# Kernel optimization log

Hardware: AMD Instinct MI355X
Metric: run time of the kernel (lower is better)

The kernel has to match this reference:

```python
import jax, jax.numpy as jnp
import numpy as np

N_LAYERS = 24
HID = 512
HEADS = 16
HEAD_DIM = HID // HEADS
CAP = 2048
VOCAB = 1025
EOS = 1024
FF = 2048
PE_LEN = 4096
EPS = 1e-5


def setup_inputs() -> dict:
    key = jax.random.key(0)
    ks = jax.random.split(key, 24)
    g = lambda k, shp, s=0.05: jax.random.normal(k, shp, jnp.float32) * s
    return {
        'last_token': jax.random.randint(ks[0], (1, 1), 0, 1024, dtype=jnp.int32),
        'position_index': jax.random.randint(ks[1], (1,), 0, 1024, dtype=jnp.int32),
        'cache_len': jax.random.randint(ks[2], (1,), 0, 1024, dtype=jnp.int32),
        'k_cache': g(ks[3], (N_LAYERS, 1, CAP, HID)),
        'v_cache': g(ks[4], (N_LAYERS, 1, CAP, HID)),
        'emb_table': g(ks[5], (VOCAB, HID)),
        'pe_table': g(ks[6], (PE_LEN, HID)),
        'x_scale': jnp.ones((1,), jnp.float32),
        'alpha': jnp.ones((1,), jnp.float32),
        'qkv_w_t': g(ks[7], (N_LAYERS, HID, 3 * HID)),
        'qkv_b': g(ks[8], (N_LAYERS, 3 * HID)),
        'out_w_t': g(ks[9], (N_LAYERS, HID, HID)),
        'out_b': g(ks[10], (N_LAYERS, HID)),
        'norm_w1': jnp.ones((N_LAYERS, HID), jnp.float32),
        'norm_b1': jnp.zeros((N_LAYERS, HID), jnp.float32),
        'norm_w2': jnp.ones((N_LAYERS, HID), jnp.float32),
        'norm_b2': jnp.zeros((N_LAYERS, HID), jnp.float32),
        'w1_t': g(ks[11], (N_LAYERS, HID, FF)),
        'b1': g(ks[12], (N_LAYERS, FF)),
        'w2_t': g(ks[13], (N_LAYERS, FF, HID)),
        'b2': g(ks[14], (N_LAYERS, HID)),
        'pred_w': g(ks[15], (VOCAB, HID)),
        'pred_b': g(ks[16], (VOCAB,)),
    }


def _layer_norm(x, w, b):
    mu = jnp.mean(x, axis=-1, keepdims=True)
    var = jnp.mean((x - mu) ** 2, axis=-1, keepdims=True)
    return (x - mu) * jax.lax.rsqrt(var + EPS) * w + b


def _decode_core(xy, cache_len, k_cache, v_cache, qkv_w_t, qkv_b, out_w_t, out_b,
                 norm_w1, norm_b1, norm_w2, norm_b2, w1_t, b1, w2_t, b2):
    B, Q, _ = xy.shape  # [1, 1, HID]
    clen = cache_len.astype(jnp.int32).reshape(1)
    next_len = clen + Q
    positions = jnp.arange(CAP)
    write_mask = (positions == clen)[None, :, None]           # [1, CAP, 1]
    valid = (positions < next_len)[None, :, None]             # [1, CAP, 1]
    inv_attn = (positions >= next_len)[None, None, None, :]   # [1, 1, 1, CAP]

    def layer(x, p):
        qw, qb, ow, ob, nw1, nb1, nw2, nb2, W1, B1, W2, B2, kc, vc = p
        qkv = x @ qw + qb                       # [B, Q, 3*HID]
        q, k, v = jnp.split(qkv, 3, axis=-1)
        # one-hot slot write + zero invalid tail (faithful to _update_cache_slot/_zero_invalid_cache_tail)
        kc = jnp.where(valid, jnp.where(write_mask, k, kc), 0.0)
        vc = jnp.where(valid, jnp.where(write_mask, v, vc), 0.0)
        qh = q.reshape(B, Q, HEADS, HEAD_DIM).transpose(0, 2, 1, 3)
        kh = kc.reshape(B, CAP, HEADS, HEAD_DIM).transpose(0, 2, 1, 3)
        vh = vc.reshape(B, CAP, HEADS, HEAD_DIM).transpose(0, 2, 1, 3)
        scores = jnp.einsum('bhqd,bhkd->bhqk', qh, kh) / jnp.sqrt(jnp.float32(HEAD_DIM))
        scores = jnp.where(inv_attn, jnp.float32(-1e30), scores)
        attn = jax.nn.softmax(scores, axis=-1)
        o = jnp.einsum('bhqk,bhkd->bhqd', attn, vh).transpose(0, 2, 1, 3).reshape(B, Q, HID)
        o = o @ ow + ob
        x = _layer_norm(x + o, nw1, nb1)
        h = jax.nn.relu(x @ W1 + B1) @ W2 + B2
        x = _layer_norm(x + h, nw2, nb2)
        return x, (kc, vc)

    x, (k_out, v_out) = jax.lax.scan(
        layer, xy,
        (qkv_w_t, qkv_b, out_w_t, out_b, norm_w1, norm_b1, norm_w2, norm_b2,
         w1_t, b1, w2_t, b2, k_cache, v_cache))
    return x, k_out, v_out, next_len


def reference(last_token, position_index, cache_len, k_cache, v_cache,
              emb_table, pe_table, x_scale, alpha,
              qkv_w_t, qkv_b, out_w_t, out_b,
              norm_w1, norm_b1, norm_w2, norm_b2,
              w1_t, b1, w2_t, b2, pred_w, pred_b):
    y_emb = emb_table[last_token]                              # [B, Q, HID]
    pos = pe_table[position_index.astype(jnp.int32)][None]     # [1, Q, HID]
    xy = y_emb * x_scale[0] + alpha[0] * pos
    x, k_out, v_out, next_len = _decode_core(
        xy, cache_len, k_cache, v_cache, qkv_w_t, qkv_b, out_w_t, out_b,
        norm_w1, norm_b1, norm_w2, norm_b2, w1_t, b1, w2_t, b2)
    logits = x[:, -1] @ pred_w.T + pred_b                      # [B, VOCAB]
    sampled = jnp.argmax(logits, axis=-1, keepdims=True).astype(jnp.int32)
    eos = (sampled.reshape(-1) == EOS).astype(jnp.int32)
    next_pos = position_index.astype(jnp.int32).reshape(1) + 1
    return (logits, sampled, eos, next_len, next_pos, k_out, v_out)
```

## Files before the change

### kernel.cpp

```cpp
#include <hip/hip_runtime.h>
#include <math.h>

#define NL     24
#define HIDDEN 512
#define H3     1536
#define HD     32
#define CAPCTX 2048
#define FFD    2048
#define NVOCAB 1025
#define GRID   256
#define NT     256
#define EPSLN  1e-5f
#define ISQ    0.17677669529663687f

__device__ __forceinline__ float gld(const float* p){ return __hip_atomic_load(p, __ATOMIC_RELAXED, __HIP_MEMORY_SCOPE_AGENT); }
__device__ __forceinline__ void  gst(float* p, float v){ __hip_atomic_store(p, v, __ATOMIC_RELAXED, __HIP_MEMORY_SCOPE_AGENT); }
__device__ __forceinline__ int   ild(const int* p){ return __hip_atomic_load(p, __ATOMIC_RELAXED, __HIP_MEMORY_SCOPE_AGENT); }
__device__ __forceinline__ void  ist(int* p, int v){ __hip_atomic_store(p, v, __ATOMIC_RELAXED, __HIP_MEMORY_SCOPE_AGENT); }

__device__ __forceinline__ void done_add(int* ctr, int tid){
  __syncthreads();
  if (tid == 0) __hip_atomic_fetch_add(ctr, 1, __ATOMIC_RELAXED, __HIP_MEMORY_SCOPE_AGENT);
}
__device__ __forceinline__ void waitge1(const int* c, int tgt){
  if (threadIdx.x == 0){
    int g = 0;
    while (__hip_atomic_load(c, __ATOMIC_RELAXED, __HIP_MEMORY_SCOPE_AGENT) < tgt){
      if (++g > (1<<25)) break;
    }
  }
  __syncthreads();
}
__device__ __forceinline__ void waitgeN(const int* base, int n, int tgt){
  if ((int)threadIdx.x < n){
    const int* c = base + threadIdx.x*16;
    int g = 0;
    while (__hip_atomic_load(c, __ATOMIC_RELAXED, __HIP_MEMORY_SCOPE_AGENT) < tgt){
      if (++g > (1<<25)) break;
    }
  }
  __syncthreads();
}
#define PIN() asm volatile("" ::: "memory")

#define KVF(kb)   ((kb)*16)
#define HEADC(h)  ((64+(h))*16)
#define FF1G(g)   ((80+(g))*16)
#define PRED_C    (88*16)
#define SLINE(par,h) ((90 + (par)*16 + (h))*16)

struct LdsF { float xn[HIDDEN]; float red[16*17]; float r8[8]; float s16[16]; float h16[16]; };
struct LdsAt{ float xn[HIDDEN]; float q[HD]; float e[128]; float v[128*33]; float red[288]; float r8[8]; float o32[HD]; };
union  Lds  { LdsF f; LdsAt a; };

__device__ __forceinline__ void bsum2(float &a, float &bb, float* lds8, int tid){
  #pragma unroll
  for (int o=32;o;o>>=1){ a += __shfl_down(a,o); bb += __shfl_down(bb,o); }
  __syncthreads();
  if ((tid&63)==0){ int w=tid>>6; lds8[w]=a; lds8[4+w]=bb; }
  __syncthreads();
  a  = lds8[0]+lds8[1]+lds8[2]+lds8[3];
  bb = lds8[4]+lds8[5]+lds8[6]+lds8[7];
  __syncthreads();
}

template<int K>
__device__ __forceinline__ float dotred(const float* w, const float* xn, float* red, int tid){
  const int c = tid & 15, s = tid >> 4;
  float a = 0.f;
  #pragma unroll
  for (int k=0;k<K;k++) a += xn[s + 16*k] * w[k];
  red[s*17 + c] = a;
  __syncthreads();
  float d = 0.f;
  if (s == 0){
    #pragma unroll
    for (int k=0;k<16;k++) d += red[k*17 + c];
  }
  __syncthreads();
  return d;
}

__device__ __forceinline__ void kvcopy(int idx, int T, int l, int clen,
    const float* __restrict__ KC, const float* __restrict__ VC,
    float* KO, float* VO, int tid){
  const int t7 = tid & 127, halfr = tid >> 7;
  const float4 z4 = make_float4(0.f,0.f,0.f,0.f);
  for (int r0 = idx*2; r0 < 4096; r0 += 2*T){
    int r = r0 + halfr;
    int p = r & 2047, isv = r >> 11;
    if (p != clen){
      float4* dst = (float4*)((isv ? VO : KO) + ((size_t)l*CAPCTX + p)*HIDDEN);
      if (p < clen){
        const float4* src = (const float4*)((isv ? VC : KC) + ((size_t)l*CAPCTX + p)*HIDDEN);
        dst[t7] = src[t7];
      } else {
        dst[t7] = z4;
      }
    }
  }
}

__global__ __launch_bounds__(NT, 1)
void t2s_decode(const int* __restrict__ LT, const int* __restrict__ PI, const int* __restrict__ CL,
                const float* __restrict__ KC, const float* __restrict__ VC,
                const float* __restrict__ EMB, const float* __restrict__ PE,
                const float* __restrict__ XSc, const float* __restrict__ ALp,
                const float* __restrict__ QKVW, const float* __restrict__ QKVB,
                const float* __restrict__ OUTW, const float* __restrict__ OUTB,
                const float* __restrict__ NW1, const float* __restrict__ NB1,
                const float* __restrict__ NW2, const float* __restrict__ NB2,
                const float* __restrict__ W1, const float* __restrict__ B1,
                const float* __restrict__ W2, const float* __restrict__ B2,
                const float* __restrict__ PW, const float* __restrict__ PB,
                float* __restrict__ OUT, float* __restrict__ WS)
{
  __shared__ Lds L;
  const int b = blockIdx.x, tid = threadIdx.x;

  int* C = (int*)WS;
  float* F   = WS + 2048;
  float* wop = F;
  float* wf2 = F + 16384;
  float* wx  = F + 24576;
  float* wx1 = F + 25088;
  float* wkv = F + 25600;

  float* KO = OUT + 1029;
  float* VO = KO + (size_t)NL*CAPCTX*HIDDEN;

  const int token = LT[0], posi = PI[0], clen = CL[0], nlen = clen + 1;
  const int nch = (nlen + 127) >> 7;
  const int T_copy = 128 + 16*(8 - nch);

  if (b >= 128){
    const int t = b - 128, h = t & 15, ci = t >> 4;
    const int cstar = clen >> 7;

    if (ci >= nch){
      const int idx = 128 + (ci - nch)*16 + h;
      for (int l=0;l<NL;l++) kvcopy(idx, T_copy, l, clen, KC, VC, KO, VO, tid);
    } else {
      const int c = tid & 31, s5 = tid >> 5;
      const int pl = tid >> 1, half = tid & 1, dbase = half << 4;
      const int p = (ci << 7) + pl;
      const bool validp = (p < nlen);
      const bool isnew  = validp && (p == clen);

      for (int l=0;l<NL;l++){
        const int par = l & 1;
        float pfQ[64];
        {
          const float* Wq = QKVW + (size_t)l*HIDDEN*H3 + (size_t)s5*H3 + h*HD + c;
          #pragma unroll
          for (int k=0;k<64;k++) pfQ[k] = Wq[(size_t)(k*8)*H3];
        }
        float qb = QKVB[(size_t)l*H3 + h*HD + c];
        float pfO[64];
        {
          const float* Wo = OUTW + (size_t)l*HIDDEN*HIDDEN + (size_t)(h*HD)*HIDDEN + tid;
          #pragma unroll
          for (int d=0;d<32;d++){ pfO[d] = Wo[(size_t)d*HIDDEN]; pfO[32+d] = Wo[(size_t)d*HIDDEN + 256]; }
        }
        float kbuf[16], vbuf[16];
        if (validp && !isnew){
          const size_t rowoff = ((size_t)l*CAPCTX + p)*HIDDEN + h*HD + dbase;
          const float4* sk = (const float4*)(KC + rowoff);
          const float4* sv = (const float4*)(VC + rowoff);
          #pragma unroll
          for (int k4=0;k4<4;k4++){
            float4 a = sk[k4];
            kbuf[4*k4]=a.x; kbuf[4*k4+1]=a.y; kbuf[4*k4+2]=a.z; kbuf[4*k4+3]=a.w;
            float4 cc = sv[k4];
            vbuf[4*k4]=cc.x; vbuf[4*k4+1]=cc.y; vbuf[4*k4+2]=cc.z; vbuf[4*k4+3]=cc.w;
          }
        }
        float lnb[2]={0,0}, lnw[2]={0,0}, lnn[2]={0,0};
        if (l > 0){
          #pragma unroll
          for (int r=0;r<2;r++){
            int i = tid + r*NT;
            lnb[r] = B2[(size_t)(l-1)*HIDDEN + i];
            lnw[r] = NW2[(size_t)(l-1)*HIDDEN + i];
            lnn[r] = NB2[(size_t)(l-1)*HIDDEN + i];
          }
        }
        PIN();

        if (l > 0) waitgeN(C + FF1G(0), 8, 16*l);

        float xn0, xn1;
        if (l == 0){
          float xs = XSc[0], al = ALp[0];
          xn0 = EMB[(size_t)token*HIDDEN + tid]*xs       + al*PE[(size_t)posi*HIDDEN + tid];
          xn1 = EMB[(size_t)token*HIDDEN + tid + 256]*xs + al*PE[(size_t)posi*HIDDEN + tid + 256];
        } else {
          float t0 = gld(&wx1[tid]) + lnb[0];
          float t1 = gld(&wx1[tid+256]) + lnb[1];
          const float* f2p = wf2 + (par^1)*4096;
          #pragma unroll
          for (int rg=0; rg<8; rg++){
            t0 += gld(&f2p[rg*512 + tid]);
            t1 += gld(&f2p[rg*512 + tid + 256]);
          }
          float s1 = t0 + t1, s2 = t0*t0 + t1*t1;
          bsum2(s1, s2, L.a.r8, tid);
          float mu = s1*(1.f/HIDDEN), rstd = rsqrtf(s2*(1.f/HIDDEN)-mu*mu+EPSLN);
          xn0 = (t0-mu)*rstd*lnw[0] + lnn[0];
          xn1 = (t1-mu)*rstd*lnw[1] + lnn[1];
        }
        L.a.xn[tid] = xn0; L.a.xn[tid+256] = xn1;
        if (b == 128){ gst(&wx[tid], xn0); gst(&wx[tid+256], xn1); }
        __syncthreads();

        {
          float qa = 0.f;
          #pragma unroll
          for (int k=0;k<64;k++) qa += L.a.xn[s5 + 8*k] * pfQ[k];
          L.a.red[s5*33 + c] = qa;
          __syncthreads();
          if (tid < 32){
            float qs = 0.f;
            #pragma unroll
            for (int k=0;k<8;k++) qs += L.a.red[k*33 + tid];
            L.a.q[tid] = (qs + qb) * ISQ;
          }
          __syncthreads();
        }

        if (ci == cstar){
          if (tid < 4){
            int kb = (tid>>1)*32 + 2*h + (tid&1);
            const int* fl = C + KVF(kb);
            int g = 0;
            while (ild(fl) < l+1){ if (++g > (1<<25)) break; }
          }
          __syncthreads();
        }

        float e = 0.f;
        if (validp){
          if (isnew){
            #pragma unroll
            for (int k=0;k<16;k++){
              kbuf[k] = gld(&wkv[h*HD + dbase + k]);
              vbuf[k] = gld(&wkv[512 + h*HD + dbase + k]);
            }
          }
          float dot = 0.f;
          #pragma unroll
          for (int k=0;k<16;k++) dot += kbuf[k] * L.a.q[dbase + k];
          dot += __shfl_xor(dot, 1);
          e = expf(dot);
        } else {
          #pragma unroll
          for (int k=0;k<16;k++) vbuf[k] = 0.f;
        }
        if (half == 0) L.a.e[pl] = validp ? e : 0.f;
        #pragma unroll
        for (int k=0;k<16;k++) L.a.v[pl*33 + dbase + k] = vbuf[k];
        __syncthreads();

        float se = (tid < 128) ? L.a.e[tid] : 0.f;
        #pragma unroll
        for (int o=32;o;o>>=1) se += __shfl_xor(se, o);
        if ((tid&63)==0) L.a.r8[tid>>6] = se;
        __syncthreads();
        const float S_ci = L.a.r8[0]+L.a.r8[1]+L.a.r8[2]+L.a.r8[3];

        {
          const int d = tid & 31, grp = tid >> 5;
          float oacc = 0.f;
          #pragma unroll
          for (int q2=0;q2<16;q2++){ int pp = (grp<<4) + q2; oacc += L.a.e[pp] * L.a.v[pp*33 + d]; }
          L.a.red[tid] = oacc;
          __syncthreads();
          if (tid < 32){
            float o8 = 0.f;
            #pragma unroll
            for (int g=0; g<8; g++) o8 += L.a.red[tid + (g<<5)];
            L.a.o32[tid] = o8;
          }
          if (tid == 0) unsafeAtomicAdd((float*)(C + SLINE(par,h)), S_ci);
          __syncthreads();
        }

        {
          float a0 = 0.f, a1 = 0.f;
          #pragma unroll
          for (int d=0; d<32; d++){ a0 += L.a.o32[d]*pfO[d]; a1 += L.a.o32[d]*pfO[32+d]; }
          unsafeAtomicAdd(&wop[par*8192 + h*512 + tid], a0);
          unsafeAtomicAdd(&wop[par*8192 + h*512 + 256 + tid], a1);
        }
        done_add(&C[HEADC(h)], tid);
      }
    }
    return;
  }

  {
    const int f = b, rgrp = f >> 4;
    const bool iskv = (f < 64);
    const int mat = f >> 5;
    const int c0  = (f & 31) << 4;

    for (int l=0;l<NL;l++){
      const int par = l & 1;
      float pfKV[32]; float pfKb = 0.f;
      float lnb[2]={0,0}, lnw[2]={0,0}, lnn[2]={0,0};
      if (iskv){
        const float* Wk = QKVW + (size_t)l*HIDDEN*H3 + (size_t)(tid>>4)*H3 + HIDDEN + mat*HIDDEN + c0 + (tid&15);
        #pragma unroll
        for (int k=0;k<32;k++) pfKV[k] = Wk[(size_t)(k*16)*H3];
        pfKb = QKVB[(size_t)l*H3 + HIDDEN + mat*HIDDEN + c0 + (tid&15)];
        if (l > 0){
          #pragma unroll
          for (int r=0;r<2;r++){
            int i = tid + r*NT;
            lnb[r] = B2[(size_t)(l-1)*HIDDEN + i];
            lnw[r] = NW2[(size_t)(l-1)*HIDDEN + i];
            lnn[r] = NB2[(size_t)(l-1)*HIDDEN + i];
          }
        }
      }
      float pfF1[32];
      {
        const float* W1p = W1 + (size_t)l*HIDDEN*FFD + (size_t)(tid>>4)*FFD + f*16 + (tid&15);
        #pragma unroll
        for (int k=0;k<32;k++) pfF1[k] = W1p[(size_t)(k*16)*FFD];
      }
      float pfF2[32];
      {
        const float* W2p = W2 + (size_t)l*FFD*HIDDEN + (size_t)(f*16)*HIDDEN + tid;
        #pragma unroll
        for (int cc=0;cc<16;cc++){ pfF2[cc] = W2p[(size_t)cc*HIDDEN]; pfF2[16+cc] = W2p[(size_t)cc*HIDDEN + 256]; }
      }
      float pfOB[2], pfW1n[2], pfB1n[2];
      #pragma unroll
      for (int r=0;r<2;r++){
        int i = tid + r*NT;
        pfOB[r]  = OUTB[(size_t)l*HIDDEN + i];
        pfW1n[r] = NW1[(size_t)l*HIDDEN + i];
        pfB1n[r] = NB1[(size_t)l*HIDDEN + i];
      }
      float pfB1f = B1[(size_t)l*FFD + f*16 + (tid&15)];
      PIN();

      if (iskv){
        if (l > 0){
          waitgeN(C + FF1G(0), 8, 16*l);
          float t0 = gld(&wx1[tid]) + lnb[0];
          float t1 = gld(&wx1[tid+256]) + lnb[1];
          const float* f2p = wf2 + (par^1)*4096;
          #pragma unroll
          for (int rg=0; rg<8; rg++){
            t0 += gld(&f2p[rg*512 + tid]);
            t1 += gld(&f2p[rg*512 + tid + 256]);
          }
          float s1 = t0 + t1, s2 = t0*t0 + t1*t1;
          bsum2(s1, s2, L.f.r8, tid);
          float mu = s1*(1.f/HIDDEN), rstd = rsqrtf(s2*(1.f/HIDDEN)-mu*mu+EPSLN);
          L.f.xn[tid]     = (t0-mu)*rstd*lnw[0] + lnn[0];
          L.f.xn[tid+256] = (t1-mu)*rstd*lnw[1] + lnn[1];
        } else {
          float xs = XSc[0], al = ALp[0];
          L.f.xn[tid]     = EMB[(size_t)token*HIDDEN + tid]*xs       + al*PE[(size_t)posi*HIDDEN + tid];
          L.f.xn[tid+256] = EMB[(size_t)token*HIDDEN + tid + 256]*xs + al*PE[(size_t)posi*HIDDEN + tid + 256];
        }
        __syncthreads();
        float dsum = dotred<32>(pfKV, L.f.xn, L.f.red, tid);
        if (tid < 16){
          int j = c0 + tid;
          float val = dsum + pfKb;
          gst(&wkv[mat*HIDDEN + j], val);
          float* dst = (mat ? VO : KO) + ((size_t)l*CAPCTX + clen)*HIDDEN + j;
          *dst = val;
        }
        __syncthreads();
        if (tid == 0) ist(&C[KVF(f)], l+1);
      }

      kvcopy(f, T_copy, l, clen, KC, VC, KO, VO, tid);

      waitgeN(C + HEADC(0), 16, nch*(l+1));

      if (tid < 64) gst(&wop[(par^1)*8192 + (f>>3)*512 + (f&7)*64 + tid], 0.f);
      if (tid < 32) gst(&wf2[(par^1)*4096 + f*32 + tid], 0.f);
      if (f < 16 && tid == 0) gst((float*)(C + SLINE(par^1, f)), 0.f);

      if (tid < 16) L.f.s16[tid] = 1.f / gld((const float*)(C + SLINE(par, tid)));
      __syncthreads();
      float t0 = gld(&wx[tid]) + pfOB[0];
      float t1 = gld(&wx[tid+256]) + pfOB[1];
      #pragma unroll
      for (int h2=0; h2<16; h2++){
        float is = L.f.s16[h2];
        t0 += gld(&wop[par*8192 + h2*512 + tid]) * is;
        t1 += gld(&wop[par*8192 + h2*512 + tid + 256]) * is;
      }
      float s1 = t0 + t1, s2 = t0*t0 + t1*t1;
      bsum2(s1, s2, L.f.r8, tid);
      float mu = s1*(1.f/HIDDEN), rstd = rsqrtf(s2*(1.f/HIDDEN)-mu*mu+EPSLN);
      float xn0 = (t0-mu)*rstd*pfW1n[0] + pfB1n[0];
      float xn1 = (t1-mu)*rstd*pfW1n[1] + pfB1n[1];
      L.f.xn[tid] = xn0; L.f.xn[tid+256] = xn1;
      if (f == 0){ gst(&wx1[tid], xn0); gst(&wx1[tid+256], xn1); }
      __syncthreads();

      float dsum = dotred<32>(pfF1, L.f.xn, L.f.red, tid);
      if (tid < 16) L.f.h16[tid] = fmaxf(dsum + pfB1f, 0.f);
      __syncthreads();
      float a0 = 0.f, a1 = 0.f;
      #pragma unroll
      for (int cc=0; cc<16; cc++){ float hv = L.f.h16[cc]; a0 += hv*pfF2[cc]; a1 += hv*pfF2[16+cc]; }
      unsafeAtomicAdd(&wf2[par*4096 + rgrp*512 + tid], a0);
      unsafeAtomicAdd(&wf2[par*4096 + rgrp*512 + 256 + tid], a1);
      done_add(&C[FF1G(rgrp)], tid);
    }

    if (f < 65){
      const int v0 = f << 4;
      const int nrows = (f == 64) ? 1 : 16;
      const int rr = tid >> 4, s2l = tid & 15;
      float pfP[32]; float pfPb = 0.f;
      if (rr < nrows){
        const float* row = PW + (size_t)(v0+rr)*HIDDEN;
        #pragma unroll
        for (int mm=0; mm<32; mm++) pfP[mm] = row[s2l + (mm<<4)];
        pfPb = PB[v0+rr];
      }
      float lnb[2], lnw[2], lnn[2];
      #pragma unroll
      for (int r=0;r<2;r++){
        int i = tid + r*NT;
        lnb[r] = B2[(size_t)(NL-1)*HIDDEN + i];
        lnw[r] = NW2[(size_t)(NL-1)*HIDDEN + i];
        lnn[r] = NB2[(size_t)(NL-1)*HIDDEN + i];
      }
      PIN();
      waitgeN(C + FF1G(0), 8, 16*NL);
      float t0 = gld(&wx1[tid]) + lnb[0];
      float t1 = gld(&wx1[tid+256]) + lnb[1];
      const float* f2p = wf2 + 4096;
      #pragma unroll
      for (int rg=0; rg<8; rg++){
        t0 += gld(&f2p[rg*512 + tid]);
        t1 += gld(&f2p[rg*512 + tid + 256]);
      }
      float s1 = t0 + t1, s2 = t0*t0 + t1*t1;
      bsum2(s1, s2, L.f.r8, tid);
      float mu = s1*(1.f/HIDDEN), rstd = rsqrtf(s2*(1.f/HIDDEN)-mu*mu+EPSLN);
      L.f.xn[tid]     = (t0-mu)*rstd*lnw[0] + lnn[0];
      L.f.xn[tid+256] = (t1-mu)*rstd*lnw[1] + lnn[1];
      __syncthreads();
      if (rr < nrows){
        float acc = 0.f;
        #pragma unroll
        for (int mm=0; mm<32; mm++) acc += L.f.xn[s2l + (mm<<4)] * pfP[mm];
        #pragma unroll
        for (int o=1;o<16;o<<=1) acc += __shfl_xor(acc, o);
        if (s2l == 0) gst(&OUT[v0+rr], acc + pfPb);
      }
      done_add(&C[PRED_C], tid);
    }

    if (b == 0){
      waitge1(&C[PRED_C], 65);
      float bv = -3.0e38f; int bi = 0;
      for (int v=tid; v<NVOCAB; v+=NT){
        float x = gld(&OUT[v]);
        if (x > bv){ bv = x; bi = v; }
      }
      L.f.xn[tid] = bv;
      ((int*)&L.f.xn[256])[tid] = bi;
      __syncthreads();
      for (int step=128; step; step>>=1){
        if (tid < step){
          float ov2 = L.f.xn[tid+step]; int oi = ((int*)&L.f.xn[256])[tid+step];
          float mv  = L.f.xn[tid];      int mi = ((int*)&L.f.xn[256])[tid];
          if (ov2 > mv || (ov2 == mv && oi < mi)){ L.f.xn[tid]=ov2; ((int*)&L.f.xn[256])[tid]=oi; }
        }
        __syncthreads();
      }
      if (tid == 0){
        int bi0 = ((int*)&L.f.xn[256])[0];
        OUT[NVOCAB]   = (float)bi0;
        OUT[NVOCAB+1] = (bi0 == 1024) ? 1.f : 0.f;
        OUT[NVOCAB+2] = (float)nlen;
        OUT[NVOCAB+3] = (float)(posi + 1);
      }
    }
  }
}

extern "C" void kernel_launch(void* const* d_in, const int* in_sizes, int n_in,
                              void* d_out, int out_size, void* d_ws, size_t ws_size,
                              hipStream_t stream) {
  (void)in_sizes; (void)n_in; (void)out_size; (void)ws_size;
  hipMemsetAsync(d_ws, 0, 8192 + 65536 + 32768, stream);
  t2s_decode<<<GRID, NT, 0, stream>>>(
    (const int*)d_in[0], (const int*)d_in[1], (const int*)d_in[2],
    (const float*)d_in[3], (const float*)d_in[4],
    (const float*)d_in[5], (const float*)d_in[6],
    (const float*)d_in[7], (const float*)d_in[8],
    (const float*)d_in[9], (const float*)d_in[10],
    (const float*)d_in[11], (const float*)d_in[12],
    (const float*)d_in[13], (const float*)d_in[14],
    (const float*)d_in[15], (const float*)d_in[16],
    (const float*)d_in[17], (const float*)d_in[18],
    (const float*)d_in[19], (const float*)d_in[20],
    (const float*)d_in[21], (const float*)d_in[22],
    (float*)d_out, (float*)d_ws);
}
```

Measured before the change: 340.8 us.

## Redistribute KV copy across all blocks, defer weight prefetches, add spin sleeps

The KV-cache copy is now spread over every block with a fixed stride, and attention blocks also do a slice of it after each layer, so the copy overlaps compute. The out-projection and FF2 weight prefetches are moved later, just before use, to ease register pressure during the waits. The softmax denominator reduction is merged into the output-accumulation barrier and one barrier is dropped from bsum2. Spin-wait loops gain s_sleep to cut atomic polling traffic, and expf becomes __expf. Risks include extra wait latency from the sleeps, LDS races from the removed barrier, and uneven copy balance.

```diff
diff --git a/kernel.cpp b/kernel.cpp
--- a/kernel.cpp
+++ b/kernel.cpp
@@ -26,7 +26,8 @@
   if (threadIdx.x == 0){
     int g = 0;
     while (__hip_atomic_load(c, __ATOMIC_RELAXED, __HIP_MEMORY_SCOPE_AGENT) < tgt){
-      if (++g > (1<<25)) break;
+      __builtin_amdgcn_s_sleep(1);
+      if (++g > (1<<24)) break;
     }
   }
   __syncthreads();
@@ -36,7 +37,8 @@
     const int* c = base + threadIdx.x*16;
     int g = 0;
     while (__hip_atomic_load(c, __ATOMIC_RELAXED, __HIP_MEMORY_SCOPE_AGENT) < tgt){
-      if (++g > (1<<25)) break;
+      __builtin_amdgcn_s_sleep(1);
+      if (++g > (1<<24)) break;
     }
   }
   __syncthreads();
@@ -61,7 +63,6 @@
   __syncthreads();
   a  = lds8[0]+lds8[1]+lds8[2]+lds8[3];
   bb = lds8[4]+lds8[5]+lds8[6]+lds8[7];
-  __syncthreads();
 }
 
 template<int K>
@@ -81,12 +82,12 @@
   return d;
 }
 
-__device__ __forceinline__ void kvcopy(int idx, int T, int l, int clen,
+__device__ __forceinline__ void kvcopy(int idx, int l, int clen,
     const float* __restrict__ KC, const float* __restrict__ VC,
     float* KO, float* VO, int tid){
   const int t7 = tid & 127, halfr = tid >> 7;
   const float4 z4 = make_float4(0.f,0.f,0.f,0.f);
-  for (int r0 = idx*2; r0 < 4096; r0 += 2*T){
+  for (int r0 = idx*2; r0 < 4096; r0 += 512){
     int r = r0 + halfr;
     int p = r & 2047, isv = r >> 11;
     if (p != clen){
@@ -131,21 +132,20 @@
 
   const int token = LT[0], posi = PI[0], clen = CL[0], nlen = clen + 1;
   const int nch = (nlen + 127) >> 7;
-  const int T_copy = 128 + 16*(8 - nch);
 
   if (b >= 128){
     const int t = b - 128, h = t & 15, ci = t >> 4;
     const int cstar = clen >> 7;
 
     if (ci >= nch){
-      const int idx = 128 + (ci - nch)*16 + h;
-      for (int l=0;l<NL;l++) kvcopy(idx, T_copy, l, clen, KC, VC, KO, VO, tid);
+      for (int l=0;l<NL;l++) kvcopy(b, l, clen, KC, VC, KO, VO, tid);
     } else {
       const int c = tid & 31, s5 = tid >> 5;
       const int pl = tid >> 1, half = tid & 1, dbase = half << 4;
       const int p = (ci << 7) + pl;
       const bool validp = (p < nlen);
       const bool isnew  = validp && (p == clen);
+      const bool iscstar = (ci == cstar);
 
       for (int l=0;l<NL;l++){
         const int par = l & 1;
@@ -156,12 +156,6 @@
           for (int k=0;k<64;k++) pfQ[k] = Wq[(size_t)(k*8)*H3];
         }
         float qb = QKVB[(size_t)l*H3 + h*HD + c];
-        float pfO[64];
-        {
-          const float* Wo = OUTW + (size_t)l*HIDDEN*HIDDEN + (size_t)(h*HD)*HIDDEN + tid;
-          #pragma unroll
-          for (int d=0;d<32;d++){ pfO[d] = Wo[(size_t)d*HIDDEN]; pfO[32+d] = Wo[(size_t)d*HIDDEN + 256]; }
-        }
         float kbuf[16], vbuf[16];
         if (validp && !isnew){
           const size_t rowoff = ((size_t)l*CAPCTX + p)*HIDDEN + h*HD + dbase;
@@ -199,9 +193,9 @@
           float t1 = gld(&wx1[tid+256]) + lnb[1];
           const float* f2p = wf2 + (par^1)*4096;
           #pragma unroll
-          for (int rg=0; rg<8; rg++){
-            t0 += gld(&f2p[rg*512 + tid]);
-            t1 += gld(&f2p[rg*512 + tid + 256]);
+          for (int g=0; g<8; g++){
+            t0 += gld(&f2p[g*512 + tid]);
+            t1 += gld(&f2p[g*512 + tid + 256]);
           }
           float s1 = t0 + t1, s2 = t0*t0 + t1*t1;
           bsum2(s1, s2, L.a.r8, tid);
@@ -228,12 +222,20 @@
           __syncthreads();
         }
 
-        if (ci == cstar){
+        float pfO[64];
+        {
+          const float* Wo = OUTW + (size_t)l*HIDDEN*HIDDEN + (size_t)(h*HD)*HIDDEN + tid;
+          #pragma unroll
+          for (int d=0;d<32;d++){ pfO[d] = Wo[(size_t)d*HIDDEN]; pfO[32+d] = Wo[(size_t)d*HIDDEN + 256]; }
+        }
+        PIN();
+
+        if (iscstar){
           if (tid < 4){
             int kb = (tid>>1)*32 + 2*h + (tid&1);
             const int* fl = C + KVF(kb);
             int g = 0;
-            while (ild(fl) < l+1){ if (++g > (1<<25)) break; }
+            while (ild(fl) < l+1){ __builtin_amdgcn_s_sleep(1); if (++g > (1<<24)) break; }
           }
           __syncthreads();
         }
@@ -251,7 +253,7 @@
           #pragma unroll
           for (int k=0;k<16;k++) dot += kbuf[k] * L.a.q[dbase + k];
           dot += __shfl_xor(dot, 1);
-          e = expf(dot);
+          e = __expf(dot);
         } else {
           #pragma unroll
           for (int k=0;k<16;k++) vbuf[k] = 0.f;
@@ -260,13 +262,6 @@
         #pragma unroll
         for (int k=0;k<16;k++) L.a.v[pl*33 + dbase + k] = vbuf[k];
         __syncthreads();
-
-        float se = (tid < 128) ? L.a.e[tid] : 0.f;
-        #pragma unroll
-        for (int o=32;o;o>>=1) se += __shfl_xor(se, o);
-        if ((tid&63)==0) L.a.r8[tid>>6] = se;
-        __syncthreads();
-        const float S_ci = L.a.r8[0]+L.a.r8[1]+L.a.r8[2]+L.a.r8[3];
 
         {
           const int d = tid & 31, grp = tid >> 5;
@@ -274,14 +269,21 @@
           #pragma unroll
           for (int q2=0;q2<16;q2++){ int pp = (grp<<4) + q2; oacc += L.a.e[pp] * L.a.v[pp*33 + d]; }
           L.a.red[tid] = oacc;
+          float se = (tid < 128) ? L.a.e[tid] : 0.f;
+          #pragma unroll
+          for (int o=32;o;o>>=1) se += __shfl_xor(se, o);
+          if ((tid&63)==0) L.a.r8[tid>>6] = se;
           __syncthreads();
+          if (tid == 0){
+            float S_ci = L.a.r8[0]+L.a.r8[1]+L.a.r8[2]+L.a.r8[3];
+            unsafeAtomicAdd((float*)(C + SLINE(par,h)), S_ci);
+          }
           if (tid < 32){
             float o8 = 0.f;
             #pragma unroll
             for (int g=0; g<8; g++) o8 += L.a.red[tid + (g<<5)];
             L.a.o32[tid] = o8;
           }
-          if (tid == 0) unsafeAtomicAdd((float*)(C + SLINE(par,h)), S_ci);
           __syncthreads();
         }
 
@@ -293,6 +295,8 @@
           unsafeAtomicAdd(&wop[par*8192 + h*512 + 256 + tid], a1);
         }
         done_add(&C[HEADC(h)], tid);
+
+        kvcopy(b, l, clen, KC, VC, KO, VO, tid);
       }
     }
     return;
@@ -328,12 +332,6 @@
         const float* W1p = W1 + (size_t)l*HIDDEN*FFD + (size_t)(tid>>4)*FFD + f*16 + (tid&15);
         #pragma unroll
         for (int k=0;k<32;k++) pfF1[k] = W1p[(size_t)(k*16)*FFD];
-      }
-      float pfF2[32];
-      {
-        const float* W2p = W2 + (size_t)l*FFD*HIDDEN + (size_t)(f*16)*HIDDEN + tid;
-        #pragma unroll
-        for (int cc=0;cc<16;cc++){ pfF2[cc] = W2p[(size_t)cc*HIDDEN]; pfF2[16+cc] = W2p[(size_t)cc*HIDDEN + 256]; }
       }
       float pfOB[2], pfW1n[2], pfB1n[2];
       #pragma unroll
@@ -353,9 +351,9 @@
           float t1 = gld(&wx1[tid+256]) + lnb[1];
           const float* f2p = wf2 + (par^1)*4096;
           #pragma unroll
-          for (int rg=0; rg<8; rg++){
-            t0 += gld(&f2p[rg*512 + tid]);
-            t1 += gld(&f2p[rg*512 + tid + 256]);
+          for (int g=0; g<8; g++){
+            t0 += gld(&f2p[g*512 + tid]);
+            t1 += gld(&f2p[g*512 + tid + 256]);
           }
           float s1 = t0 + t1, s2 = t0*t0 + t1*t1;
           bsum2(s1, s2, L.f.r8, tid);
@@ -380,7 +378,7 @@
         if (tid == 0) ist(&C[KVF(f)], l+1);
       }
 
-      kvcopy(f, T_copy, l, clen, KC, VC, KO, VO, tid);
+      kvcopy(b, l, clen, KC, VC, KO, VO, tid);
 
       waitgeN(C + HEADC(0), 16, nch*(l+1));
 
@@ -407,9 +405,29 @@
       if (f == 0){ gst(&wx1[tid], xn0); gst(&wx1[tid+256], xn1); }
       __syncthreads();
 
-      float dsum = dotred<32>(pfF1, L.f.xn, L.f.red, tid);
-      if (tid < 16) L.f.h16[tid] = fmaxf(dsum + pfB1f, 0.f);
-      __syncthreads();
+      float pfF2[32];
+      {
+        const float* W2p = W2 + (size_t)l*FFD*HIDDEN + (size_t)(f*16)*HIDDEN + tid;
+        #pragma unroll
+        for (int cc=0;cc<16;cc++){ pfF2[cc] = W2p[(size_t)cc*HIDDEN]; pfF2[16+cc] = W2p[(size_t)cc*HIDDEN + 256]; }
+      }
+      PIN();
+
+      {
+        const int cc = tid & 15, s = tid >> 4;
+        float a = 0.f;
+        #pragma unroll
+        for (int k=0;k<32;k++) a += L.f.xn[s + 16*k] * pfF1[k];
+        L.f.red[s*17 + cc] = a;
+        __syncthreads();
+        if (tid < 16){
+          float dd = 0.f;
+          #pragma unroll
+          for (int k=0;k<16;k++) dd += L.f.red[k*17 + tid];
+          L.f.h16[tid] = fmaxf(dd + pfB1f, 0.f);
+        }
+        __syncthreads();
+      }
       float a0 = 0.f, a1 = 0.f;
       #pragma unroll
       for (int cc=0; cc<16; cc++){ float hv = L.f.h16[cc]; a0 += hv*pfF2[cc]; a1 += hv*pfF2[16+cc]; }
@@ -443,9 +461,9 @@
       float t1 = gld(&wx1[tid+256]) + lnb[1];
       const float* f2p = wf2 + 4096;
       #pragma unroll
-      for (int rg=0; rg<8; rg++){
-        t0 += gld(&f2p[rg*512 + tid]);
-        t1 += gld(&f2p[rg*512 + tid + 256]);
+      for (int g=0; g<8; g++){
+        t0 += gld(&f2p[g*512 + tid]);
+        t1 += gld(&f2p[g*512 + tid + 256]);
       }
       float s1 = t0 + t1, s2 = t0*t0 + t1*t1;
       bsum2(s1, s2, L.f.r8, tid);
```

Measured after the change: 347.3 us. About the same (+1.9%).
